# Kernel optimization log

Hardware: AMD Instinct MI355X
Metric: run time of the kernel (lower is better)

## Reference

```python
import jax, jax.numpy as jnp
import numpy as np

V, D, T_MAX, H, L = 32000, 1024, 1024, 16, 8
HD = D // H
DFF = 4 * D
EPS = 1e-5


def _pos_encoding(T, d_model, dtype=jnp.float32):
    pos = jnp.arange(T, dtype=jnp.float32)[:, None]                      # [T,1]
    div = jnp.exp(jnp.arange(0, d_model, 2, dtype=jnp.float32) * (-jnp.log(10000.0) / d_model))
    pe = jnp.zeros((T, d_model), dtype=jnp.float32)
    pe = pe.at[:, 0::2].set(jnp.sin(pos * div))
    pe = pe.at[:, 1::2].set(jnp.cos(pos * div))
    return pe.astype(dtype)


def _layernorm(x, g, b):
    mu = jnp.mean(x, axis=-1, keepdims=True)
    var = jnp.mean(jnp.square(x - mu), axis=-1, keepdims=True)
    return (x - mu) * jax.lax.rsqrt(var + EPS) * g + b


def setup_inputs() -> dict:
    key = jax.random.key(0)
    ks = jax.random.split(key, 9)
    s = 0.02
    return {
        "idx": jax.random.randint(ks[0], (2, 1024), 0, V),
        "embed": jax.random.normal(ks[1], (V, D), jnp.float32) * s,
        "Wqkv": jax.random.normal(ks[2], (L, D, 3 * D), jnp.float32) * s,
        "Wproj": jax.random.normal(ks[3], (L, D, D), jnp.float32) * s,
        "bproj": jnp.zeros((L, D), jnp.float32),
        "ln1_g": jnp.ones((L, D), jnp.float32),
        "ln1_b": jnp.zeros((L, D), jnp.float32),
        "ln2_g": jnp.ones((L, D), jnp.float32),
        "ln2_b": jnp.zeros((L, D), jnp.float32),
        "W1": jax.random.normal(ks[4], (L, D, DFF), jnp.float32) * s,
        "b1": jnp.zeros((L, DFF), jnp.float32),
        "W2": jax.random.normal(ks[5], (L, DFF, D), jnp.float32) * s,
        "b2": jnp.zeros((L, D), jnp.float32),
        "lnf_g": jnp.ones((D,), jnp.float32),
        "lnf_b": jnp.zeros((D,), jnp.float32),
        "Whead": jax.random.normal(ks[6], (D, V), jnp.float32) * s,
    }


def _attn(x, Wqkv, Wproj, bproj):
    B, T, C = x.shape
    qkv = (x @ Wqkv).reshape(B, T, 3, H, HD)
    q, k, v = [jnp.transpose(qkv[:, :, i], (0, 2, 1, 3)) for i in range(3)]  # [B,H,T,HD]
    scores = jnp.einsum('bhqd,bhkd->bhqk', q, k) * (HD ** -0.5)
    mask = jnp.tril(jnp.ones((T, T), dtype=bool))
    scores = jnp.where(mask, scores, -jnp.inf)
    w = jax.nn.softmax(scores, axis=-1)
    out = jnp.einsum('bhqk,bhkd->bhqd', w, v)
    out = jnp.transpose(out, (0, 2, 1, 3)).reshape(B, T, C)
    return out @ Wproj + bproj


def reference(idx, embed, Wqkv, Wproj, bproj, ln1_g, ln1_b, ln2_g, ln2_b,
              W1, b1, W2, b2, lnf_g, lnf_b, Whead):
    idx = idx[:, :T_MAX]
    T = idx.shape[1]
    x = embed[idx] + _pos_encoding(T, D)[None]          # [B,T,D]
    for l in range(L):
        x = x + _attn(_layernorm(x, ln1_g[l], ln1_b[l]), Wqkv[l], Wproj[l], bproj[l])
        h = _layernorm(x, ln2_g[l], ln2_b[l])
        x = x + jax.nn.relu(h @ W1[l] + b1[l]) @ W2[l] + b2[l]
    x = _layernorm(x, lnf_g, lnf_b)
    return x @ Whead                                     # [B,T,V]
```

## Files before the change

### kernel.cpp

```cpp
#include <hip/hip_runtime.h>
#include <cstddef>

#define DM    1024
#define TSEQ  1024
#define NB    2
#define NHEAD 16
#define HDIM  64
#define NLAYER 8
#define DFFN  4096
#define NVOC  32000
#define NROWS (NB*TSEQ)

typedef __attribute__((ext_vector_type(8))) short short8;
typedef __attribute__((ext_vector_type(4))) float f32x4;

static __device__ __forceinline__ unsigned short f2bf(float f) {
    union { float f; unsigned int u; } v; v.f = f;
    unsigned int r = v.u + 0x7FFF + ((v.u >> 16) & 1);
    return (unsigned short)(r >> 16);
}

static __device__ __forceinline__ void gload_lds16(const void* g, void* l) {
    __builtin_amdgcn_global_load_lds(
        (const __attribute__((address_space(1))) unsigned int*)g,
        (__attribute__((address_space(3))) unsigned int*)l, 16, 0, 0);
}

__global__ __launch_bounds__(256)
void embed_pos_k(const int* __restrict__ idx, const float* __restrict__ embed,
                 float* __restrict__ x)
{
    int row = blockIdx.x;
    int t   = row & (TSEQ - 1);
    int tid = threadIdx.x;
    int token = idx[row];
    const float* er = embed + (size_t)token * DM;
    float* xr = x + (size_t)row * DM;
    const float neg_ln1e4_over_d = -9.210340371976184f / (float)DM;
    for (int i = tid; i < DM; i += 256) {
        int half = i >> 1;
        float div = expf((float)(2 * half) * neg_ln1e4_over_d);
        float ang = (float)t * div;
        float pe = (i & 1) ? cosf(ang) : sinf(ang);
        xr[i] = er[i] + pe;
    }
}

__global__ __launch_bounds__(256)
void layernorm_k(const float* __restrict__ x, const float* __restrict__ g,
                 const float* __restrict__ b, unsigned short* __restrict__ y)
{
    int row = blockIdx.x;
    int tid = threadIdx.x;
    const float* xr = x + (size_t)row * DM;
    unsigned short* yr = y + (size_t)row * DM;
    float vals[4];
    float s = 0.f;
    #pragma unroll
    for (int i = 0; i < 4; ++i) { vals[i] = xr[tid + 256 * i]; s += vals[i]; }
    __shared__ float red[256];
    red[tid] = s; __syncthreads();
    for (int st = 128; st > 0; st >>= 1) {
        if (tid < st) red[tid] += red[tid + st];
        __syncthreads();
    }
    float mu = red[0] * (1.f / DM);
    __syncthreads();
    float v = 0.f;
    #pragma unroll
    for (int i = 0; i < 4; ++i) { float d = vals[i] - mu; v += d * d; }
    red[tid] = v; __syncthreads();
    for (int st = 128; st > 0; st >>= 1) {
        if (tid < st) red[tid] += red[tid + st];
        __syncthreads();
    }
    float rstd = rsqrtf(red[0] * (1.f / DM) + 1e-5f);
    #pragma unroll
    for (int i = 0; i < 4; ++i) {
        int c = tid + 256 * i;
        yr[c] = f2bf((vals[i] - mu) * rstd * g[c] + b[c]);
    }
}

__global__ __launch_bounds__(256)
void reduce_ln_k(const float* __restrict__ P, int nsplit, const float* __restrict__ bias,
                 float* __restrict__ X, const float* __restrict__ g,
                 const float* __restrict__ b, unsigned short* __restrict__ XN)
{
    const int row = blockIdx.x;
    const int tid = threadIdx.x;
    const size_t off4 = (size_t)row * 256 + tid;
    const size_t tot4 = (size_t)NROWS * 256;

    float4 v = *((const float4*)X + off4);
    float4 bb = *((const float4*)bias + tid);
    v.x += bb.x; v.y += bb.y; v.z += bb.z; v.w += bb.w;
    for (int s = 0; s < nsplit; ++s) {
        float4 p = *((const float4*)P + s * tot4 + off4);
        v.x += p.x; v.y += p.y; v.z += p.z; v.w += p.w;
    }
    *((float4*)X + off4) = v;

    __shared__ float red[256];
    red[tid] = v.x + v.y + v.z + v.w;
    __syncthreads();
    for (int st = 128; st > 0; st >>= 1) {
        if (tid < st) red[tid] += red[tid + st];
        __syncthreads();
    }
    float mu = red[0] * (1.f / DM);
    __syncthreads();
    float4 d = make_float4(v.x - mu, v.y - mu, v.z - mu, v.w - mu);
    red[tid] = d.x * d.x + d.y * d.y + d.z * d.z + d.w * d.w;
    __syncthreads();
    for (int st = 128; st > 0; st >>= 1) {
        if (tid < st) red[tid] += red[tid + st];
        __syncthreads();
    }
    float rstd = rsqrtf(red[0] * (1.f / DM) + 1e-5f);
    float4 gg = *((const float4*)g + tid);
    float4 bbn = *((const float4*)b + tid);
    unsigned short o[4];
    o[0] = f2bf(d.x * rstd * gg.x + bbn.x);
    o[1] = f2bf(d.y * rstd * gg.y + bbn.y);
    o[2] = f2bf(d.z * rstd * gg.z + bbn.z);
    o[3] = f2bf(d.w * rstd * gg.w + bbn.w);
    *(ushort4*)(XN + (size_t)row * DM + tid * 4) = *(ushort4*)o;
}

__global__ __launch_bounds__(256)
void convt_k(const float* __restrict__ src, unsigned short* __restrict__ dst,
             int K, int N)
{
    __shared__ __align__(16) unsigned short T[64][72];
    const int tid = threadIdx.x;
    const int n0 = blockIdx.x * 64, k0 = blockIdx.y * 64;
    const float* s = src + (size_t)blockIdx.z * K * N;
    unsigned short* d = dst + (size_t)blockIdx.z * K * N;
    #pragma unroll
    for (int q = 0; q < 4; ++q) {
        int f4 = tid + q * 256;
        int kk = f4 >> 4, nn = (f4 & 15) * 4;
        float4 v = *(const float4*)(s + (size_t)(k0 + kk) * N + n0 + nn);
        int swz = ((nn >> 2) & 7) << 3;
        T[nn + 0][kk ^ swz] = f2bf(v.x);
        T[nn + 1][kk ^ swz] = f2bf(v.y);
        T[nn + 2][kk ^ swz] = f2bf(v.z);
        T[nn + 3][kk ^ swz] = f2bf(v.w);
    }
    __syncthreads();
    #pragma unroll
    for (int q = 0; q < 2; ++q) {
        int s8 = tid + q * 256;
        int nn = s8 >> 3, kc = (s8 & 7) * 8;
        int swz = ((nn >> 2) & 7) << 3;
        *(short8*)(d + (size_t)(n0 + nn) * K + k0 + kc) =
            *(const short8*)&T[nn][kc ^ swz];
    }
}

template<bool OUT_BF16>
__global__ __launch_bounds__(512)
void gemm256(const unsigned short* __restrict__ A, const unsigned short* __restrict__ BT,
             const float* __restrict__ bias, void* __restrict__ Cout,
             int M, int N, int K, int relu)
{
    __shared__ __align__(16) unsigned short AS[3][256][64];
    __shared__ __align__(16) unsigned short BS[3][128][64];

    const int tid  = threadIdx.x;
    const int lane = tid & 63;
    const int w    = tid >> 6;
    const int wm = w >> 1, wn = w & 1;
    const int l16 = lane & 15, g = lane >> 4;

    const int nby = M / 256;
    const int nwg = nby * (N / 128);
    const int cpx = nwg >> 3;
    const int bid = (int)blockIdx.x;
    const int sbid = (bid & 7) * cpx + (bid >> 3);
    const int row0 = (sbid % nby) * 256;
    const int col0 = (sbid / nby) * 128;

    const int srow = tid >> 3;
    const int schunk = ((tid & 7) ^ (srow & 7)) << 3;
    const unsigned short* ga = A  + (size_t)(row0 + srow) * K + schunk;
    const unsigned short* gb = BT + (size_t)(col0 + srow) * K + schunk;
    const int NT = K >> 6;

    const int ch0 = ((g ^ (l16 & 7)) << 3);
    const int ch1 = (((4 | g) ^ (l16 & 7)) << 3);
    const int ar0 = wm * 64 + 0  + l16;
    const int ar1 = wm * 64 + 16 + l16;
    const int ar2 = wm * 64 + 32 + l16;
    const int ar3 = wm * 64 + 48 + l16;
    const int br0 = wn * 64 + 0  + l16;
    const int br1 = wn * 64 + 16 + l16;
    const int br2 = wn * 64 + 32 + l16;
    const int br3 = wn * 64 + 48 + l16;

    f32x4 acc[4][4] = {};

    #pragma unroll
    for (int t = 0; t < 2; ++t) {
        #pragma unroll
        for (int i = 0; i < 4; ++i)
            gload_lds16(ga + t * 64 + (size_t)(i * 64) * K,
                        (unsigned short*)AS[t] + i * 4096 + tid * 8);
        #pragma unroll
        for (int i = 0; i < 2; ++i)
            gload_lds16(gb + t * 64 + (size_t)(i * 64) * K,
                        (unsigned short*)BS[t] + i * 4096 + tid * 8);
    }
    asm volatile("s_waitcnt vmcnt(6)" ::: "memory");
    __builtin_amdgcn_s_barrier();

    short8 aE0 = *(const short8*)&AS[0][ar0][ch0];
    short8 aE1 = *(const short8*)&AS[0][ar1][ch0];
    short8 aO0, aO1;
    short8 b0f[4], b1f[4];
    b0f[0] = *(const short8*)&BS[0][br0][ch0];
    b0f[1] = *(const short8*)&BS[0][br1][ch0];
    b0f[2] = *(const short8*)&BS[0][br2][ch0];
    b0f[3] = *(const short8*)&BS[0][br3][ch0];

    for (int t = 0; t < NT; ++t) {
        const int rs = t % 3;
        const int ss = (t + 2) % 3;
        const bool pf = (t + 2 < NT);
        const unsigned short* gat = ga + (t + 2) * 64;
        const unsigned short* gbt = gb + (t + 2) * 64;

        aO0 = *(const short8*)&AS[rs][ar2][ch0];
        aO1 = *(const short8*)&AS[rs][ar3][ch0];
        if (pf) {
            gload_lds16(gat,                      (unsigned short*)AS[ss] + 0 * 4096 + tid * 8);
            gload_lds16(gat + (size_t)64 * K,     (unsigned short*)AS[ss] + 1 * 4096 + tid * 8);
        }
        __builtin_amdgcn_s_setprio(1);
        #pragma unroll
        for (int j = 0; j < 4; ++j)
            acc[0][j] = __builtin_amdgcn_mfma_f32_16x16x32_bf16(aE0, b0f[j], acc[0][j], 0, 0, 0);
        #pragma unroll
        for (int j = 0; j < 4; ++j)
            acc[1][j] = __builtin_amdgcn_mfma_f32_16x16x32_bf16(aE1, b0f[j], acc[1][j], 0, 0, 0);
        __builtin_amdgcn_s_setprio(0);
        __builtin_amdgcn_s_barrier();

        aE0 = *(const short8*)&AS[rs][ar0][ch1];
        aE1 = *(const short8*)&AS[rs][ar1][ch1];
        b1f[0] = *(const short8*)&BS[rs][br0][ch1];
        b1f[1] = *(const short8*)&BS[rs][br1][ch1];
        b1f[2] = *(const short8*)&BS[rs][br2][ch1];
        b1f[3] = *(const short8*)&BS[rs][br3][ch1];
        if (pf) {
            gload_lds16(gat + (size_t)128 * K,    (unsigned short*)AS[ss] + 2 * 4096 + tid * 8);
            gload_lds16(gat + (size_t)192 * K,    (unsigned short*)AS[ss] + 3 * 4096 + tid * 8);
        }
        __builtin_amdgcn_s_setprio(1);
        #pragma unroll
        for (int j = 0; j < 4; ++j)
            acc[2][j] = __builtin_amdgcn_mfma_f32_16x16x32_bf16(aO0, b0f[j], acc[2][j], 0, 0, 0);
        #pragma unroll
        for (int j = 0; j < 4; ++j)
            acc[3][j] = __builtin_amdgcn_mfma_f32_16x16x32_bf16(aO1, b0f[j], acc[3][j], 0, 0, 0);
        __builtin_amdgcn_s_setprio(0);
        __builtin_amdgcn_s_barrier();

        aO0 = *(const short8*)&AS[rs][ar2][ch1];
        aO1 = *(const short8*)&AS[rs][ar3][ch1];
        if (pf)
            gload_lds16(gbt,                      (unsigned short*)BS[ss] + 0 * 4096 + tid * 8);
        __builtin_amdgcn_s_setprio(1);
        #pragma unroll
        for (int j = 0; j < 4; ++j)
            acc[0][j] = __builtin_amdgcn_mfma_f32_16x16x32_bf16(aE0, b1f[j], acc[0][j], 0, 0, 0);
        #pragma unroll
        for (int j = 0; j < 4; ++j)
            acc[1][j] = __builtin_amdgcn_mfma_f32_16x16x32_bf16(aE1, b1f[j], acc[1][j], 0, 0, 0);
        __builtin_amdgcn_s_setprio(0);
        __builtin_amdgcn_s_barrier();

        if (pf)
            gload_lds16(gbt + (size_t)64 * K,     (unsigned short*)BS[ss] + 1 * 4096 + tid * 8);
        __builtin_amdgcn_s_setprio(1);
        #pragma unroll
        for (int j = 0; j < 4; ++j)
            acc[2][j] = __builtin_amdgcn_mfma_f32_16x16x32_bf16(aO0, b1f[j], acc[2][j], 0, 0, 0);
        #pragma unroll
        for (int j = 0; j < 4; ++j)
            acc[3][j] = __builtin_amdgcn_mfma_f32_16x16x32_bf16(aO1, b1f[j], acc[3][j], 0, 0, 0);
        __builtin_amdgcn_s_setprio(0);
        if (pf) { asm volatile("s_waitcnt vmcnt(6)" ::: "memory"); }
        else    { asm volatile("s_waitcnt vmcnt(0)" ::: "memory"); }
        __builtin_amdgcn_s_barrier();

        if (t + 1 < NT) {
            const int rs2 = (t + 1) % 3;
            aE0 = *(const short8*)&AS[rs2][ar0][ch0];
            aE1 = *(const short8*)&AS[rs2][ar1][ch0];
            b0f[0] = *(const short8*)&BS[rs2][br0][ch0];
            b0f[1] = *(const short8*)&BS[rs2][br1][ch0];
            b0f[2] = *(const short8*)&BS[rs2][br2][ch0];
            b0f[3] = *(const short8*)&BS[rs2][br3][ch0];
        }
    }

    #pragma unroll
    for (int i = 0; i < 4; ++i) {
        #pragma unroll
        for (int j = 0; j < 4; ++j) {
            #pragma unroll
            for (int r = 0; r < 4; ++r) {
                int row = row0 + wm * 64 + i * 16 + g * 4 + r;
                int col = col0 + wn * 64 + j * 16 + l16;
                float v = acc[i][j][r];
                if (bias) v += bias[col];
                if (relu) v = fmaxf(v, 0.f);
                if (OUT_BF16) ((unsigned short*)Cout)[(size_t)row * N + col] = f2bf(v);
                else          ((float*)Cout)[(size_t)row * N + col] = v;
            }
        }
    }
}

template<int BM, bool OUT_BF16>
__global__ __launch_bounds__(256)
void gemm_tn(const unsigned short* __restrict__ A, const unsigned short* __restrict__ BT,
             const float* __restrict__ bias, const float* __restrict__ residual,
             void* __restrict__ Cout, int M, int N, int K, int KS, int relu)
{
    constexpr int FR = BM / 32;
    constexpr int RPW = BM / 4;
    constexpr int NI = BM / 64;
    __shared__ __align__(16) unsigned short As[2][BM][32];
    __shared__ __align__(16) unsigned short Bs[2][BM][32];

    const int tid = threadIdx.x;
    const int lane = tid & 63;
    const int w = tid >> 6;
    const int wr = w >> 1, wc = w & 1;
    const int l16 = lane & 15, g = lane >> 4;

    const int nby = M / BM;
    const int nwg = (N / BM) * nby;
    const int cpx = nwg >> 3;
    const int bid = blockIdx.x;
    const int sbid = (bid & 7) * cpx + (bid >> 3);
    const int row0 = (sbid % nby) * BM;
    const int col0 = (sbid / nby) * BM;

    const int srow = w * RPW + (lane >> 2);
    const int scol = (((lane & 3) ^ ((lane >> 3) & 3)) << 3);
    const int rslot = ((g ^ ((l16 >> 1) & 3)) << 3);

    const unsigned short* ga = A  + (size_t)(row0 + srow) * KS + (size_t)blockIdx.y * K + scol;
    const unsigned short* gb = BT + (size_t)(col0 + srow) * KS + (size_t)blockIdx.y * K + scol;

    f32x4 acc[FR][FR] = {};

    #pragma unroll
    for (int i = 0; i < NI; ++i) {
        gload_lds16(ga + (size_t)(i * 16) * KS, &As[0][srow + i * 16][(lane & 3) << 3]);
        gload_lds16(gb + (size_t)(i * 16) * KS, &Bs[0][srow + i * 16][(lane & 3) << 3]);
    }
    __syncthreads();

    int cur = 0;
    for (int k0 = 0; k0 < K; k0 += 32) {
        if (k0 + 32 < K) {
            #pragma unroll
            for (int i = 0; i < NI; ++i) {
                gload_lds16(ga + k0 + 32 + (size_t)(i * 16) * KS, &As[cur ^ 1][srow + i * 16][(lane & 3) << 3]);
                gload_lds16(gb + k0 + 32 + (size_t)(i * 16) * KS, &Bs[cur ^ 1][srow + i * 16][(lane & 3) << 3]);
            }
        }
        short8 af[FR], bf[FR];
        #pragma unroll
        for (int i = 0; i < FR; ++i)
            af[i] = *(const short8*)&As[cur][wr * (BM / 2) + i * 16 + l16][rslot];
        #pragma unroll
        for (int j = 0; j < FR; ++j)
            bf[j] = *(const short8*)&Bs[cur][wc * (BM / 2) + j * 16 + l16][rslot];
        #pragma unroll
        for (int i = 0; i < FR; ++i)
            #pragma unroll
            for (int j = 0; j < FR; ++j)
                acc[i][j] = __builtin_amdgcn_mfma_f32_16x16x32_bf16(af[i], bf[j], acc[i][j], 0, 0, 0);
        __syncthreads();
        cur ^= 1;
    }

    float* Cf = (float*)Cout + (size_t)blockIdx.y * M * N;
    #pragma unroll
    for (int i = 0; i < FR; ++i) {
        #pragma unroll
        for (int j = 0; j < FR; ++j) {
            #pragma unroll
            for (int r = 0; r < 4; ++r) {
                int row = row0 + wr * (BM / 2) + i * 16 + g * 4 + r;
                int col = col0 + wc * (BM / 2) + j * 16 + l16;
                float v = acc[i][j][r];
                if (bias)     v += bias[col];
                if (residual) v += residual[(size_t)row * N + col];
                if (relu)     v = fmaxf(v, 0.f);
                if (OUT_BF16) ((unsigned short*)Cout)[(size_t)row * N + col] = f2bf(v);
                else          Cf[(size_t)row * N + col] = v;
            }
        }
    }
}

__global__ __launch_bounds__(256)
void attn_flash_k(const unsigned short* __restrict__ qkv, unsigned short* __restrict__ out)
{
    __shared__ unsigned short Ks[64][72];
    __shared__ unsigned short Vt[64][72];
    __shared__ unsigned short Ps[4][16][72];

    const int tid = threadIdx.x;
    const int lane = tid & 63;
    const int w = tid >> 6;
    const int l16 = lane & 15, g = lane >> 4;
    const int h = blockIdx.y;
    const int b = blockIdx.z;

    const size_t rstr = 3 * DM;
    const unsigned short* base = qkv + (size_t)b * TSEQ * rstr + h * HDIM;

    const int krow0 = tid >> 3, kcol = (tid & 7) * 8;
    const int vkv = tid & 63, vdg = tid >> 6;

    short8 kreg0, kreg1, vreg0, vreg1;

    #pragma unroll
    for (int pass = 0; pass < 2; ++pass) {
        const int qb = pass ? (15 - (int)blockIdx.x) : (int)blockIdx.x;
        const int q0 = qb * 64;
        const int nt = qb + 1;

        const int qrow_w = q0 + w * 16 + l16;
        short8 aq0 = *(const short8*)(base + (size_t)qrow_w * rstr + g * 8);
        short8 aq1 = *(const short8*)(base + (size_t)qrow_w * rstr + 32 + g * 8);

        f32x4 acc_o[4] = {};
        float m_r[4] = {-INFINITY, -INFINITY, -INFINITY, -INFINITY};
        float l_r[4] = {};

        {
            const unsigned short* kb = base + DM;
            kreg0 = *(const short8*)(kb + (size_t)krow0 * rstr + kcol);
            kreg1 = *(const short8*)(kb + (size_t)(32 + krow0) * rstr + kcol);
            const unsigned short* vsrc = base + (size_t)vkv * rstr + 2 * DM + vdg * 16;
            vreg0 = *(const short8*)vsrc;
            vreg1 = *(const short8*)(vsrc + 8);
        }

        for (int t = 0; t < nt; ++t) {
            *(short8*)&Ks[krow0][kcol] = kreg0;
            *(short8*)&Ks[32 + krow0][kcol] = kreg1;
            #pragma unroll
            for (int j = 0; j < 8; ++j) Vt[vdg * 16 + j][vkv] = (unsigned short)vreg0[j];
            #pragma unroll
            for (int j = 0; j < 8; ++j) Vt[vdg * 16 + 8 + j][vkv] = (unsigned short)vreg1[j];
            __syncthreads();

            if (t + 1 < nt) {
                const int kv0n = (t + 1) * 64;
                const unsigned short* kb = base + (size_t)kv0n * rstr + DM;
                kreg0 = *(const short8*)(kb + (size_t)krow0 * rstr + kcol);
                kreg1 = *(const short8*)(kb + (size_t)(32 + krow0) * rstr + kcol);
                const unsigned short* vsrc = base + (size_t)(kv0n + vkv) * rstr + 2 * DM + vdg * 16;
                vreg0 = *(const short8*)vsrc;
                vreg1 = *(const short8*)(vsrc + 8);
            }

            const int kv0 = t * 64;
            f32x4 acc_s[4] = {};
            #pragma unroll
            for (int ks = 0; ks < 4; ++ks) {
                short8 bk0 = *(const short8*)&Ks[ks * 16 + l16][g * 8];
                short8 bk1 = *(const short8*)&Ks[ks * 16 + l16][32 + g * 8];
                acc_s[ks] = __builtin_amdgcn_mfma_f32_16x16x32_bf16(aq0, bk0, acc_s[ks], 0, 0, 0);
                acc_s[ks] = __builtin_amdgcn_mfma_f32_16x16x32_bf16(aq1, bk1, acc_s[ks], 0, 0, 0);
            }
            const bool need_mask = (kv0 + 63 > q0 + w * 16);
            float alpha[4];
            #pragma unroll
            for (int r = 0; r < 4; ++r) {
                const int q_abs = q0 + w * 16 + g * 4 + r;
                float s[4];
                #pragma unroll
                for (int ks = 0; ks < 4; ++ks) {
                    s[ks] = acc_s[ks][r] * 0.125f;
                    if (need_mask && (kv0 + ks * 16 + l16 > q_abs)) s[ks] = -INFINITY;
                }
                float pm = fmaxf(fmaxf(s[0], s[1]), fmaxf(s[2], s[3]));
                #pragma unroll
                for (int msk = 1; msk <= 8; msk <<= 1)
                    pm = fmaxf(pm, __shfl_xor(pm, msk));
                float mnew = fmaxf(m_r[r], pm);
                alpha[r] = __expf(m_r[r] - mnew);
                m_r[r] = mnew;
                float p[4], psum = 0.f;
                #pragma unroll
                for (int ks = 0; ks < 4; ++ks) {
                    p[ks] = (s[ks] == -INFINITY) ? 0.f : __expf(s[ks] - mnew);
                    psum += p[ks];
                }
                #pragma unroll
                for (int msk = 1; msk <= 8; msk <<= 1)
                    psum += __shfl_xor(psum, msk);
                l_r[r] = l_r[r] * alpha[r] + psum;
                #pragma unroll
                for (int ks = 0; ks < 4; ++ks)
                    Ps[w][g * 4 + r][ks * 16 + l16] = f2bf(p[ks]);
            }
            #pragma unroll
            for (int ds = 0; ds < 4; ++ds)
                #pragma unroll
                for (int r = 0; r < 4; ++r)
                    acc_o[ds][r] *= alpha[r];
            short8 ap0 = *(const short8*)&Ps[w][l16][g * 8];
            short8 ap1 = *(const short8*)&Ps[w][l16][32 + g * 8];
            #pragma unroll
            for (int ds = 0; ds < 4; ++ds) {
                short8 bv0 = *(const short8*)&Vt[ds * 16 + l16][g * 8];
                short8 bv1 = *(const short8*)&Vt[ds * 16 + l16][32 + g * 8];
                acc_o[ds] = __builtin_amdgcn_mfma_f32_16x16x32_bf16(ap0, bv0, acc_o[ds], 0, 0, 0);
                acc_o[ds] = __builtin_amdgcn_mfma_f32_16x16x32_bf16(ap1, bv1, acc_o[ds], 0, 0, 0);
            }
            __syncthreads();
        }

        #pragma unroll
        for (int ds = 0; ds < 4; ++ds)
            #pragma unroll
            for (int r = 0; r < 4; ++r) {
                int row = q0 + w * 16 + g * 4 + r;
                out[((size_t)b * TSEQ + row) * DM + h * HDIM + ds * 16 + l16] =
                    f2bf(acc_o[ds][r] * (1.f / l_r[r]));
            }
    }
}

extern "C" void kernel_launch(void* const* d_in, const int* in_sizes, int n_in,
                              void* d_out, int out_size, void* d_ws, size_t ws_size,
                              hipStream_t stream)
{
    const int*   idx    = (const int*)  d_in[0];
    const float* embed  = (const float*)d_in[1];
    const float* Wqkv   = (const float*)d_in[2];
    const float* Wproj  = (const float*)d_in[3];
    const float* bproj  = (const float*)d_in[4];
    const float* ln1_g  = (const float*)d_in[5];
    const float* ln1_b  = (const float*)d_in[6];
    const float* ln2_g  = (const float*)d_in[7];
    const float* ln2_b  = (const float*)d_in[8];
    const float* W1     = (const float*)d_in[9];
    const float* b1     = (const float*)d_in[10];
    const float* W2     = (const float*)d_in[11];
    const float* b2     = (const float*)d_in[12];
    const float* lnf_g  = (const float*)d_in[13];
    const float* lnf_b  = (const float*)d_in[14];
    const float* Whead  = (const float*)d_in[15];
    float* out = (float*)d_out;

    float* X = (float*)d_ws;
    float* PK = X + (size_t)NROWS * DM;
    unsigned short* u = (unsigned short*)(PK + (size_t)4 * NROWS * DM);
    unsigned short* XN     = u;  u += (size_t)NROWS * DM;
    unsigned short* QKVb   = u;  u += (size_t)NROWS * 3 * DM;
    unsigned short* ATT    = u;  u += (size_t)NROWS * DM;
    unsigned short* FFH    = u;  u += (size_t)NROWS * DFFN;
    unsigned short* WqkvT  = u;  u += (size_t)NLAYER * 3 * DM * DM;
    unsigned short* WprojT = u;  u += (size_t)NLAYER * DM * DM;
    unsigned short* W1T    = u;  u += (size_t)NLAYER * DFFN * DM;
    unsigned short* W2T    = u;  u += (size_t)NLAYER * DM * DFFN;
    unsigned short* WheadT = u;  u += (size_t)NVOC * DM;

    convt_k<<<dim3(3 * DM / 64, DM / 64, NLAYER), 256, 0, stream>>>(Wqkv,  WqkvT,  DM,   3 * DM);
    convt_k<<<dim3(DM / 64,     DM / 64, NLAYER), 256, 0, stream>>>(Wproj, WprojT, DM,   DM);
    convt_k<<<dim3(DFFN / 64,   DM / 64, NLAYER), 256, 0, stream>>>(W1,    W1T,    DM,   DFFN);
    convt_k<<<dim3(DM / 64,   DFFN / 64, NLAYER), 256, 0, stream>>>(W2,    W2T,    DFFN, DM);
    convt_k<<<dim3(NVOC / 64,   DM / 64, 1),      256, 0, stream>>>(Whead, WheadT, DM,   NVOC);

    embed_pos_k<<<NROWS, 256, 0, stream>>>(idx, embed, X);
    layernorm_k<<<NROWS, 256, 0, stream>>>(X, ln1_g, ln1_b, XN);

    for (int l = 0; l < NLAYER; ++l) {
        const unsigned short* wqkvT_l  = WqkvT  + (size_t)l * 3 * DM * DM;
        const unsigned short* wprojT_l = WprojT + (size_t)l * DM * DM;
        const unsigned short* w1T_l    = W1T    + (size_t)l * DFFN * DM;
        const unsigned short* w2T_l    = W2T    + (size_t)l * DM * DFFN;
        const float* bproj_l = bproj + (size_t)l * DM;
        const float* b1_l = b1 + (size_t)l * DFFN;
        const float* b2_l = b2 + (size_t)l * DM;

        {
            int nwg = (NROWS / 256) * (3 * DM / 128);
            gemm256<true><<<nwg, 512, 0, stream>>>(XN, wqkvT_l, nullptr,
                                                   QKVb, NROWS, 3 * DM, DM, 0);
        }
        {
            dim3 grid(TSEQ / 128, NHEAD, NB);
            attn_flash_k<<<grid, 256, 0, stream>>>(QKVb, ATT);
        }
        {
            dim3 grid((NROWS / 128) * (DM / 128), 2);
            gemm_tn<128, false><<<grid, 256, 0, stream>>>(ATT, wprojT_l, nullptr, nullptr,
                                                          PK, NROWS, DM, 512, DM, 0);
            reduce_ln_k<<<NROWS, 256, 0, stream>>>(PK, 2, bproj_l, X,
                                                   ln2_g + (size_t)l * DM,
                                                   ln2_b + (size_t)l * DM, XN);
        }
        {
            int nwg = (NROWS / 256) * (DFFN / 128);
            gemm256<true><<<nwg, 512, 0, stream>>>(XN, w1T_l, b1_l,
                                                   FFH, NROWS, DFFN, DM, 1);
        }
        {
            dim3 grid((NROWS / 128) * (DM / 128), 4);
            gemm_tn<128, false><<<grid, 256, 0, stream>>>(FFH, w2T_l, nullptr, nullptr,
                                                          PK, NROWS, DM, 1024, DFFN, 0);
            const float* ng = (l + 1 < NLAYER) ? ln1_g + (size_t)(l + 1) * DM : lnf_g;
            const float* nb = (l + 1 < NLAYER) ? ln1_b + (size_t)(l + 1) * DM : lnf_b;
            reduce_ln_k<<<NROWS, 256, 0, stream>>>(PK, 4, b2_l, X, ng, nb, XN);
        }
    }

    {
        int nwg = (NROWS / 256) * (NVOC / 128);
        gemm256<false><<<nwg, 512, 0, stream>>>(XN, WheadT, nullptr,
                                                out, NROWS, NVOC, DM, 0);
    }
}
```

Baseline: 1.807 ms.

## Triple-buffer gemm_tn with one barrier per step and use it for LM head

```diff
diff --git a/kernel.cpp b/kernel.cpp
--- a/kernel.cpp
+++ b/kernel.cpp
@@ -159,6 +159,101 @@
     }
 }
 
+template<int BM, bool OUT_BF16>
+__global__ __launch_bounds__(256)
+void gemm_tn(const unsigned short* __restrict__ A, const unsigned short* __restrict__ BT,
+             const float* __restrict__ bias, const float* __restrict__ residual,
+             void* __restrict__ Cout, int M, int N, int K, int KS, int relu)
+{
+    constexpr int FR = BM / 32;
+    constexpr int RPW = BM / 4;
+    constexpr int NI = BM / 64;
+    __shared__ __align__(16) unsigned short As[3][BM][32];
+    __shared__ __align__(16) unsigned short Bs[3][BM][32];
+
+    const int tid = threadIdx.x;
+    const int lane = tid & 63;
+    const int w = tid >> 6;
+    const int wr = w >> 1, wc = w & 1;
+    const int l16 = lane & 15, g = lane >> 4;
+
+    const int nby = M / BM;
+    const int nwg = (N / BM) * nby;
+    const int cpx = nwg >> 3;
+    const int bid = blockIdx.x;
+    const int sbid = (bid & 7) * cpx + (bid >> 3);
+    const int row0 = (sbid % nby) * BM;
+    const int col0 = (sbid / nby) * BM;
+
+    const int srow = w * RPW + (lane >> 2);
+    const int scol = (((lane & 3) ^ ((lane >> 3) & 3)) << 3);
+    const int rslot = ((g ^ ((l16 >> 1) & 3)) << 3);
+    const int ldst = (lane & 3) << 3;
+
+    const unsigned short* ga = A  + (size_t)(row0 + srow) * KS + (size_t)blockIdx.y * K + scol;
+    const unsigned short* gb = BT + (size_t)(col0 + srow) * KS + (size_t)blockIdx.y * K + scol;
+
+    f32x4 acc[FR][FR] = {};
+    const int NT = K >> 5;
+
+    #pragma unroll
+    for (int i = 0; i < NI; ++i) {
+        gload_lds16(ga + (size_t)(i * 16) * KS, &As[0][srow + i * 16][ldst]);
+        gload_lds16(gb + (size_t)(i * 16) * KS, &Bs[0][srow + i * 16][ldst]);
+    }
+
+    for (int t = 0; t < NT; ++t) {
+        const int rb = t % 3;
+        if (t + 1 < NT) {
+            const int wb2 = (t + 1) % 3;
+            const int ko = (t + 1) * 32;
+            #pragma unroll
+            for (int i = 0; i < NI; ++i) {
+                gload_lds16(ga + ko + (size_t)(i * 16) * KS, &As[wb2][srow + i * 16][ldst]);
+                gload_lds16(gb + ko + (size_t)(i * 16) * KS, &Bs[wb2][srow + i * 16][ldst]);
+            }
+            asm volatile("s_waitcnt vmcnt(4)" ::: "memory");
+        } else {
+            asm volatile("s_waitcnt vmcnt(0)" ::: "memory");
+        }
+        __builtin_amdgcn_s_barrier();
+
+        short8 af[FR], bf[FR];
+        #pragma unroll
+        for (int i = 0; i < FR; ++i)
+            af[i] = *(const short8*)&As[rb][wr * (BM / 2) + i * 16 + l16][rslot];
+        #pragma unroll
+        for (int j = 0; j < FR; ++j)
+            bf[j] = *(const short8*)&Bs[rb][wc * (BM / 2) + j * 16 + l16][rslot];
+        __builtin_amdgcn_s_setprio(1);
+        #pragma unroll
+        for (int i = 0; i < FR; ++i)
+            #pragma unroll
+            for (int j = 0; j < FR; ++j)
+                acc[i][j] = __builtin_amdgcn_mfma_f32_16x16x32_bf16(af[i], bf[j], acc[i][j], 0, 0, 0);
+        __builtin_amdgcn_s_setprio(0);
+    }
+
+    float* Cf = (float*)Cout + (size_t)blockIdx.y * M * N;
+    #pragma unroll
+    for (int i = 0; i < FR; ++i) {
+        #pragma unroll
+        for (int j = 0; j < FR; ++j) {
+            #pragma unroll
+            for (int r = 0; r < 4; ++r) {
+                int row = row0 + wr * (BM / 2) + i * 16 + g * 4 + r;
+                int col = col0 + wc * (BM / 2) + j * 16 + l16;
+                float v = acc[i][j][r];
+                if (bias)     v += bias[col];
+                if (residual) v += residual[(size_t)row * N + col];
+                if (relu)     v = fmaxf(v, 0.f);
+                if (OUT_BF16) ((unsigned short*)Cout)[(size_t)row * N + col] = f2bf(v);
+                else          Cf[(size_t)row * N + col] = v;
+            }
+        }
+    }
+}
+
 template<bool OUT_BF16>
 __global__ __launch_bounds__(512)
 void gemm256(const unsigned short* __restrict__ A, const unsigned short* __restrict__ BT,
@@ -319,93 +414,6 @@
                 if (relu) v = fmaxf(v, 0.f);
                 if (OUT_BF16) ((unsigned short*)Cout)[(size_t)row * N + col] = f2bf(v);
                 else          ((float*)Cout)[(size_t)row * N + col] = v;
-            }
-        }
-    }
-}
-
-template<int BM, bool OUT_BF16>
-__global__ __launch_bounds__(256)
-void gemm_tn(const unsigned short* __restrict__ A, const unsigned short* __restrict__ BT,
-             const float* __restrict__ bias, const float* __restrict__ residual,
-             void* __restrict__ Cout, int M, int N, int K, int KS, int relu)
-{
-    constexpr int FR = BM / 32;
-    constexpr int RPW = BM / 4;
-    constexpr int NI = BM / 64;
-    __shared__ __align__(16) unsigned short As[2][BM][32];
-    __shared__ __align__(16) unsigned short Bs[2][BM][32];
-
-    const int tid = threadIdx.x;
-    const int lane = tid & 63;
-    const int w = tid >> 6;
-    const int wr = w >> 1, wc = w & 1;
-    const int l16 = lane & 15, g = lane >> 4;
-
-    const int nby = M / BM;
-    const int nwg = (N / BM) * nby;
-    const int cpx = nwg >> 3;
-    const int bid = blockIdx.x;
-    const int sbid = (bid & 7) * cpx + (bid >> 3);
-    const int row0 = (sbid % nby) * BM;
-    const int col0 = (sbid / nby) * BM;
-
-    const int srow = w * RPW + (lane >> 2);
-    const int scol = (((lane & 3) ^ ((lane >> 3) & 3)) << 3);
-    const int rslot = ((g ^ ((l16 >> 1) & 3)) << 3);
-
-    const unsigned short* ga = A  + (size_t)(row0 + srow) * KS + (size_t)blockIdx.y * K + scol;
-    const unsigned short* gb = BT + (size_t)(col0 + srow) * KS + (size_t)blockIdx.y * K + scol;
-
-    f32x4 acc[FR][FR] = {};
-
-    #pragma unroll
-    for (int i = 0; i < NI; ++i) {
-        gload_lds16(ga + (size_t)(i * 16) * KS, &As[0][srow + i * 16][(lane & 3) << 3]);
-        gload_lds16(gb + (size_t)(i * 16) * KS, &Bs[0][srow + i * 16][(lane & 3) << 3]);
-    }
-    __syncthreads();
-
-    int cur = 0;
-    for (int k0 = 0; k0 < K; k0 += 32) {
-        if (k0 + 32 < K) {
-            #pragma unroll
-            for (int i = 0; i < NI; ++i) {
-                gload_lds16(ga + k0 + 32 + (size_t)(i * 16) * KS, &As[cur ^ 1][srow + i * 16][(lane & 3) << 3]);
-                gload_lds16(gb + k0 + 32 + (size_t)(i * 16) * KS, &Bs[cur ^ 1][srow + i * 16][(lane & 3) << 3]);
-            }
-        }
-        short8 af[FR], bf[FR];
-        #pragma unroll
-        for (int i = 0; i < FR; ++i)
-            af[i] = *(const short8*)&As[cur][wr * (BM / 2) + i * 16 + l16][rslot];
-        #pragma unroll
-        for (int j = 0; j < FR; ++j)
-            bf[j] = *(const short8*)&Bs[cur][wc * (BM / 2) + j * 16 + l16][rslot];
-        #pragma unroll
-        for (int i = 0; i < FR; ++i)
-            #pragma unroll
-            for (int j = 0; j < FR; ++j)
-                acc[i][j] = __builtin_amdgcn_mfma_f32_16x16x32_bf16(af[i], bf[j], acc[i][j], 0, 0, 0);
-        __syncthreads();
-        cur ^= 1;
-    }
-
-    float* Cf = (float*)Cout + (size_t)blockIdx.y * M * N;
-    #pragma unroll
-    for (int i = 0; i < FR; ++i) {
-        #pragma unroll
-        for (int j = 0; j < FR; ++j) {
-            #pragma unroll
-            for (int r = 0; r < 4; ++r) {
-                int row = row0 + wr * (BM / 2) + i * 16 + g * 4 + r;
-                int col = col0 + wc * (BM / 2) + j * 16 + l16;
-                float v = acc[i][j][r];
-                if (bias)     v += bias[col];
-                if (residual) v += residual[(size_t)row * N + col];
-                if (relu)     v = fmaxf(v, 0.f);
-                if (OUT_BF16) ((unsigned short*)Cout)[(size_t)row * N + col] = f2bf(v);
-                else          Cf[(size_t)row * N + col] = v;
             }
         }
     }
@@ -630,8 +638,8 @@
     }
 
     {
-        int nwg = (NROWS / 256) * (NVOC / 128);
-        gemm256<false><<<nwg, 512, 0, stream>>>(XN, WheadT, nullptr,
-                                                out, NROWS, NVOC, DM, 0);
-    }
-}
+        int nwg = (NROWS / 128) * (NVOC / 128);
+        gemm_tn<128, false><<<nwg, 256, 0, stream>>>(XN, WheadT, nullptr, nullptr,
+                                                     out, NROWS, NVOC, DM, DM, 0);
+    }
+}
```

Result: faster. 1.736 ms (-3.9%).
